# Optimization experiments

Measured on AMD Instinct MI355X. Metric: run time of the kernel, lower is better.

Reference implementation:

```python
import jax, jax.numpy as jnp
import numpy as np

NEG_BIG = -9e15
LRELU_SLOPE = 0.2  # torch LeakyReLU default used for act_att


def setup_inputs() -> dict:
    key = jax.random.key(0)
    k1, k2, k3, k4 = jax.random.split(key, 4)
    B, N, F_in, F_out = 8, 2048, 128, 64
    inp = jax.random.normal(k1, (B, N, F_in), dtype=jnp.float32)
    adj = jax.random.randint(k2, (N, N), 0, 2, dtype=jnp.int32)
    W = jax.random.normal(k3, (F_in, F_out), dtype=jnp.float32) * (1.0 / np.sqrt(F_in))
    a = jax.random.normal(k4, (2 * F_out, 1), dtype=jnp.float32) * (1.0 / np.sqrt(2 * F_out))
    return {"input": inp, "adj": adj, "W": W, "a": a}


def reference(input, adj, W, a):
    # h: [B, N, F_out]
    h = jnp.einsum('bnf,fo->bno', input, W)
    F_out = W.shape[1]
    a1 = a[:F_out, 0]   # [F_out] -- applied to source node i
    a2 = a[F_out:, 0]   # [F_out] -- applied to target node j
    # e[b,i,j] = leaky_relu(h_i . a1 + h_j . a2); equivalent to cat([h_i,h_j]) @ a
    s1 = h @ a1          # [B, N]
    s2 = h @ a2          # [B, N]
    e = jax.nn.leaky_relu(s1[:, :, None] + s2[:, None, :], negative_slope=LRELU_SLOPE)
    masked = jnp.where(adj[None, :, :] > 0, e, NEG_BIG)
    attention = jax.nn.softmax(masked, axis=-1)  # [B, N, N]
    # dropout p=0.0 (eval) -> identity
    h_prime = jnp.einsum('bij,bjo->bio', attention, h)
    out = jax.nn.relu(h_prime)  # concat=True -> apply act_gat
    return out, attention[..., None]
```

## Files before the change

kernel.cpp:

```cpp
#include <hip/hip_runtime.h>
#include <hip/hip_bf16.h>

constexpr int B = 8, N = 2048, FIN = 128, FOUT = 64;

typedef __attribute__((ext_vector_type(8))) short short8;
typedef __attribute__((ext_vector_type(4))) float f32x4;

__device__ __forceinline__ unsigned int pk_bf16(float lo, float hi) {
    union { __hip_bfloat162 h2; unsigned int u; } c;
    c.h2 = __float22bfloat162_rn(float2{lo, hi});
    return c.u;
}
__device__ __forceinline__ unsigned short f2bf(float f) {
    return (unsigned short)(pk_bf16(f, 0.f) & 0xFFFFu);
}

__global__ __launch_bounds__(512, 2) void kA(
        const float* __restrict__ inp, const float* __restrict__ W,
        const float* __restrict__ a, const int* __restrict__ adj,
        unsigned short* __restrict__ hP, float* __restrict__ s1,
        float* __restrict__ s2, unsigned long long* __restrict__ adjbits) {
    __shared__ float wa1l[128], wa2l[128];
    __shared__ unsigned short wT[64][136];
    __shared__ unsigned short aT[128][136];

    int bx = blockIdx.x, t = threadIdx.x, w = t >> 6, lane = t & 63;

    if (bx >= 128) {
        int row = (bx - 128) * 8 + w;
        const int* ar = adj + (size_t)row * N;
        unsigned long long* br = adjbits + (size_t)row * 32;
        #pragma unroll 8
        for (int wq = 0; wq < 32; ++wq) {
            unsigned long long m = __ballot(ar[wq * 64 + lane] > 0);
            if (lane == 0) br[wq] = m;
        }
        return;
    }

    int b = bx >> 4, i0 = (bx & 15) * 128;

    if (t < 128) {
        const float* wr = W + t * FOUT;
        float acc1 = 0.f;
        #pragma unroll 16
        for (int o = 0; o < 64; ++o) acc1 = fmaf(wr[o], a[o], acc1);
        wa1l[t] = acc1;
    } else if (t < 256) {
        int k = t - 128;
        const float* wr = W + k * FOUT;
        float acc2 = 0.f;
        #pragma unroll 16
        for (int o = 0; o < 64; ++o) acc2 = fmaf(wr[o], a[64 + o], acc2);
        wa2l[k] = acc2;
    } else {
        int t2 = t - 256;
        int o = t2 & 63, kg = t2 >> 6;
        #pragma unroll 8
        for (int kk = 0; kk < 32; ++kk) {
            int k = kg * 32 + kk;
            wT[o][k] = f2bf(W[k * FOUT + o]);
        }
    }
    __syncthreads();

    {
        int row = t >> 2, seg = t & 3;
        const float* ip = inp + ((size_t)b * N + i0 + row) * FIN + seg * 32;
        float s1p = 0.f, s2p = 0.f;
        #pragma unroll
        for (int q = 0; q < 8; ++q) {
            float4 v = *(const float4*)&ip[q * 4];
            int k = seg * 32 + q * 4;
            s1p += v.x * wa1l[k] + v.y * wa1l[k + 1] + v.z * wa1l[k + 2] + v.w * wa1l[k + 3];
            s2p += v.x * wa2l[k] + v.y * wa2l[k + 1] + v.z * wa2l[k + 2] + v.w * wa2l[k + 3];
            unsigned int* dst = (unsigned int*)&aT[row][k];
            dst[0] = pk_bf16(v.x, v.y);
            dst[1] = pk_bf16(v.z, v.w);
        }
        s1p += __shfl_xor(s1p, 1); s1p += __shfl_xor(s1p, 2);
        s2p += __shfl_xor(s2p, 1); s2p += __shfl_xor(s2p, 2);
        if (seg == 0) {
            s1[(size_t)b * N + i0 + row] = s1p;
            s2[(size_t)b * N + i0 + row] = s2p;
        }
    }
    __syncthreads();

    int r = lane & 15, g = lane >> 4;
    int mloc = w * 16;
    f32x4 acc[4];
    #pragma unroll
    for (int nf = 0; nf < 4; ++nf)
        #pragma unroll
        for (int q = 0; q < 4; ++q) acc[nf][q] = 0.f;
    #pragma unroll
    for (int ks = 0; ks < 4; ++ks) {
        short8 Af = *(const short8*)&aT[mloc + r][ks * 32 + g * 8];
        #pragma unroll
        for (int nf = 0; nf < 4; ++nf) {
            short8 Bf = *(const short8*)&wT[nf * 16 + r][ks * 32 + g * 8];
            acc[nf] = __builtin_amdgcn_mfma_f32_16x16x32_bf16(Af, Bf, acc[nf], 0, 0, 0);
        }
    }
    __syncthreads();

    #pragma unroll
    for (int nf = 0; nf < 4; ++nf)
        #pragma unroll
        for (int q = 0; q < 4; ++q)
            aT[mloc + g * 4 + q][nf * 16 + r] = f2bf(acc[nf][q]);
    __syncthreads();

    #pragma unroll
    for (int half = 0; half < 2; ++half) {
        int idx = t + half * 512;
        int kb_l = idx >> 8, nf = (idx >> 6) & 3, ln = idx & 63;
        int g2 = ln >> 4, r2 = ln & 15;
        union { short8 s8; unsigned short u[8]; } tw;
        #pragma unroll
        for (int e = 0; e < 8; ++e)
            tw.u[e] = aT[kb_l * 32 + g2 * 8 + e][nf * 16 + r2];
        int kbg = (bx & 15) * 4 + kb_l;
        *(short8*)&hP[((((size_t)b * 64 + kbg) * 4 + nf) << 9) + ln * 8] = tw.s8;
    }
}

__global__ __launch_bounds__(512, 8) void k2a_pv(
        const float* __restrict__ s1g, const float* __restrict__ s2g,
        const unsigned long long* __restrict__ adjbits,
        const unsigned short* __restrict__ hP,
        float* __restrict__ rvg, float* __restrict__ out) {
    __shared__ float s2l[N];
    __shared__ float s1l[16];
    __shared__ float ps[8][16];
    __shared__ float rvl[16];
    __shared__ float red[7][16][68];

    int b = blockIdx.y, m0 = blockIdx.x * 16;
    int t = threadIdx.x, kc = t >> 6, lane = t & 63;
    int r = lane & 15, g = lane >> 4;

    { int j = t * 4; *(float4*)&s2l[j] = *(const float4*)&s2g[(size_t)b * N + j]; }
    if (t < 16) s1l[t] = s1g[(size_t)b * N + m0 + t];
    __syncthreads();

    float s1v = s1l[r];
    const unsigned long long* brow = adjbits + (size_t)(m0 + r) * 32 + kc * 4;
    const unsigned short* hpb = hP + (size_t)b * 64 * 4 * 512;

    f32x4 acc[4];
    #pragma unroll
    for (int nf = 0; nf < 4; ++nf)
        #pragma unroll
        for (int q = 0; q < 4; ++q) acc[nf][q] = 0.f;
    float rsum = 0.f;

    #pragma unroll
    for (int st = 0; st < 8; ++st) {
        int jb = kc * 256 + st * 32 + g * 8;
        unsigned int bits = (unsigned int)(brow[st >> 1] >> ((st & 1) * 32 + g * 8)) & 0xFFu;
        float4 sA = *(const float4*)&s2l[jb];
        float4 sB = *(const float4*)&s2l[jb + 4];
        float sj[8] = {sA.x, sA.y, sA.z, sA.w, sB.x, sB.y, sB.z, sB.w};
        float e8[8];
        #pragma unroll
        for (int e = 0; e < 8; ++e) {
            float x = s1v + sj[e];
            x = fmaxf(x, 0.2f * x);
            float pe = __expf(x);
            e8[e] = ((bits >> e) & 1u) ? pe : 0.f;
            rsum += e8[e];
        }
        union { short8 s8; unsigned int d[4]; } pk;
        #pragma unroll
        for (int e = 0; e < 4; ++e) pk.d[e] = pk_bf16(e8[2 * e], e8[2 * e + 1]);
        int kb = kc * 8 + st;
        const unsigned short* hs = hpb + (((size_t)kb * 4) << 9) + lane * 8;
        #pragma unroll
        for (int nf = 0; nf < 4; ++nf) {
            short8 Bf = *(const short8*)&hs[nf << 9];
            acc[nf] = __builtin_amdgcn_mfma_f32_16x16x32_bf16(pk.s8, Bf, acc[nf], 0, 0, 0);
        }
    }
    rsum += __shfl_xor(rsum, 16);
    rsum += __shfl_xor(rsum, 32);
    if (lane < 16) ps[kc][r] = rsum;
    if (kc > 0) {
        #pragma unroll
        for (int nf = 0; nf < 4; ++nf)
            #pragma unroll
            for (int q = 0; q < 4; ++q)
                red[kc - 1][4 * g + q][nf * 16 + r] = acc[nf][q];
    }
    __syncthreads();
    if (t < 16) {
        float rv = 1.0f / (ps[0][t] + ps[1][t] + ps[2][t] + ps[3][t]
                         + ps[4][t] + ps[5][t] + ps[6][t] + ps[7][t]);
        rvl[t] = rv;
        rvg[(size_t)b * N + m0 + t] = rv;
    }
    __syncthreads();
    if (kc == 0) {
        #pragma unroll
        for (int nf = 0; nf < 4; ++nf) {
            #pragma unroll
            for (int q = 0; q < 4; ++q) {
                int m = 4 * g + q;
                int o = nf * 16 + r;
                float vv = acc[nf][q];
                #pragma unroll
                for (int z = 0; z < 7; ++z) vv += red[z][m][o];
                vv *= rvl[m];
                out[((size_t)b * N + m0 + m) * FOUT + o] = vv > 0.f ? vv : 0.f;
            }
        }
    }
}

__global__ __launch_bounds__(256, 8) void k2b_att(
        const float* __restrict__ s1g, const float* __restrict__ s2g,
        const unsigned long long* __restrict__ adjbits,
        const float* __restrict__ rvg, float* __restrict__ att) {
    int i = blockIdx.x;
    int t = threadIdx.x, w = t >> 6, lane = t & 63;
    int b = blockIdx.y * 4 + w;
    const unsigned long long* brow = adjbits + (size_t)i * 32;
    float s1v = s1g[(size_t)b * N + i];
    float rv  = rvg[(size_t)b * N + i];
    const float* s2b = s2g + (size_t)b * N;
    float* orow = att + ((size_t)b * N + i) * N;
    #pragma unroll
    for (int it = 0; it < 8; ++it) {
        int j = it * 256 + lane * 4;
        unsigned int bits = (unsigned int)(brow[j >> 6] >> (j & 63)) & 0xFu;
        float4 sv = *(const float4*)&s2b[j];
        float x0 = s1v + sv.x; x0 = fmaxf(x0, 0.2f * x0);
        float x1 = s1v + sv.y; x1 = fmaxf(x1, 0.2f * x1);
        float x2 = s1v + sv.z; x2 = fmaxf(x2, 0.2f * x2);
        float x3 = s1v + sv.w; x3 = fmaxf(x3, 0.2f * x3);
        float4 o;
        o.x = (bits & 1u) ? __expf(x0) * rv : 0.f;
        o.y = (bits & 2u) ? __expf(x1) * rv : 0.f;
        o.z = (bits & 4u) ? __expf(x2) * rv : 0.f;
        o.w = (bits & 8u) ? __expf(x3) * rv : 0.f;
        *(float4*)&orow[j] = o;
    }
}

extern "C" void kernel_launch(void* const* d_in, const int* in_sizes, int n_in,
                              void* d_out, int out_size, void* d_ws, size_t ws_size,
                              hipStream_t stream) {
    const float* inp = (const float*)d_in[0];
    const int*   adj = (const int*)d_in[1];
    const float* W   = (const float*)d_in[2];
    const float* a   = (const float*)d_in[3];

    float* out = (float*)d_out;
    float* att = out + (size_t)B * N * FOUT;

    unsigned short* hP = (unsigned short*)d_ws;
    float* s1  = (float*)(hP + (size_t)B * FOUT * N);
    float* s2  = s1 + (size_t)B * N;
    float* rvg = s2 + (size_t)B * N;
    unsigned long long* adjbits = (unsigned long long*)(rvg + (size_t)B * N);

    kA<<<384, 512, 0, stream>>>(inp, W, a, adj, hP, s1, s2, adjbits);
    dim3 g2a(N / 16, B);
    k2a_pv<<<g2a, 512, 0, stream>>>(s1, s2, adjbits, hP, rvg, out);
    dim3 g2b(N, 2);
    k2b_att<<<g2b, 256, 0, stream>>>(s1, s2, adjbits, rvg, att);
}
```

Before: 63.41 us.

## Merge PV and attention-write kernels into one interleaved launch, recomputing row sums

The separate PV and attention-materialisation kernels are combined into one launch of 3072 blocks. Two of every three blocks write attention rows; each computes its own softmax denominator with a first pass of exp over the row before writing, so it no longer depends on the PV kernel's reciprocal. The third block in each group does the PV MFMA work. This removes a launch and the rvg dependency and lets the store-bound attention writes overlap the compute-bound PV, at the cost of computing exp twice per attention element.

Measured after the change: 86.35 us. 36.2% more time.

```diff
diff --git a/kernel.cpp b/kernel.cpp
--- a/kernel.cpp
+++ b/kernel.cpp
@@ -126,19 +126,67 @@
     }
 }
 
-__global__ __launch_bounds__(512, 8) void k2a_pv(
+__global__ __launch_bounds__(512, 8) void k2(
         const float* __restrict__ s1g, const float* __restrict__ s2g,
         const unsigned long long* __restrict__ adjbits,
         const unsigned short* __restrict__ hP,
-        float* __restrict__ rvg, float* __restrict__ out) {
+        float* __restrict__ att, float* __restrict__ out) {
     __shared__ float s2l[N];
     __shared__ float s1l[16];
     __shared__ float ps[8][16];
     __shared__ float rvl[16];
     __shared__ float red[7][16][68];
 
-    int b = blockIdx.y, m0 = blockIdx.x * 16;
-    int t = threadIdx.x, kc = t >> 6, lane = t & 63;
+    int bx = blockIdx.x;
+    int t = threadIdx.x, w = t >> 6, lane = t & 63;
+
+    if (bx % 3 != 2) {
+        int i = (bx / 3) * 2 + (bx % 3);
+        int b = w;
+        const unsigned long long* brow = adjbits + (size_t)i * 32;
+        float s1v = s1g[(size_t)b * N + i];
+        const float* s2b = s2g + (size_t)b * N;
+        float* orow = att + ((size_t)b * N + i) * N;
+        float rsum = 0.f;
+        #pragma unroll
+        for (int it = 0; it < 8; ++it) {
+            int j = it * 256 + lane * 4;
+            unsigned int bits = (unsigned int)(brow[j >> 6] >> (j & 63)) & 0xFu;
+            float4 sv = *(const float4*)&s2b[j];
+            float x0 = s1v + sv.x; x0 = fmaxf(x0, 0.2f * x0);
+            float x1 = s1v + sv.y; x1 = fmaxf(x1, 0.2f * x1);
+            float x2 = s1v + sv.z; x2 = fmaxf(x2, 0.2f * x2);
+            float x3 = s1v + sv.w; x3 = fmaxf(x3, 0.2f * x3);
+            rsum += (bits & 1u) ? __expf(x0) : 0.f;
+            rsum += (bits & 2u) ? __expf(x1) : 0.f;
+            rsum += (bits & 4u) ? __expf(x2) : 0.f;
+            rsum += (bits & 8u) ? __expf(x3) : 0.f;
+        }
+        #pragma unroll
+        for (int off = 1; off < 64; off <<= 1) rsum += __shfl_xor(rsum, off);
+        float rv = 1.0f / rsum;
+        #pragma unroll
+        for (int it = 0; it < 8; ++it) {
+            int j = it * 256 + lane * 4;
+            unsigned int bits = (unsigned int)(brow[j >> 6] >> (j & 63)) & 0xFu;
+            float4 sv = *(const float4*)&s2b[j];
+            float x0 = s1v + sv.x; x0 = fmaxf(x0, 0.2f * x0);
+            float x1 = s1v + sv.y; x1 = fmaxf(x1, 0.2f * x1);
+            float x2 = s1v + sv.z; x2 = fmaxf(x2, 0.2f * x2);
+            float x3 = s1v + sv.w; x3 = fmaxf(x3, 0.2f * x3);
+            float4 o;
+            o.x = (bits & 1u) ? __expf(x0) * rv : 0.f;
+            o.y = (bits & 2u) ? __expf(x1) * rv : 0.f;
+            o.z = (bits & 4u) ? __expf(x2) * rv : 0.f;
+            o.w = (bits & 8u) ? __expf(x3) * rv : 0.f;
+            *(float4*)&orow[j] = o;
+        }
+        return;
+    }
+
+    int pvi = bx / 3;
+    int b = pvi >> 7, m0 = (pvi & 127) * 16;
+    int kc = w;
     int r = lane & 15, g = lane >> 4;
 
     { int j = t * 4; *(float4*)&s2l[j] = *(const float4*)&s2g[(size_t)b * N + j]; }
@@ -194,12 +242,9 @@
                 red[kc - 1][4 * g + q][nf * 16 + r] = acc[nf][q];
     }
     __syncthreads();
-    if (t < 16) {
-        float rv = 1.0f / (ps[0][t] + ps[1][t] + ps[2][t] + ps[3][t]
-                         + ps[4][t] + ps[5][t] + ps[6][t] + ps[7][t]);
-        rvl[t] = rv;
-        rvg[(size_t)b * N + m0 + t] = rv;
-    }
+    if (t < 16)
+        rvl[t] = 1.0f / (ps[0][t] + ps[1][t] + ps[2][t] + ps[3][t]
+                       + ps[4][t] + ps[5][t] + ps[6][t] + ps[7][t]);
     __syncthreads();
     if (kc == 0) {
         #pragma unroll
@@ -218,36 +263,6 @@
     }
 }
 
-__global__ __launch_bounds__(256, 8) void k2b_att(
-        const float* __restrict__ s1g, const float* __restrict__ s2g,
-        const unsigned long long* __restrict__ adjbits,
-        const float* __restrict__ rvg, float* __restrict__ att) {
-    int i = blockIdx.x;
-    int t = threadIdx.x, w = t >> 6, lane = t & 63;
-    int b = blockIdx.y * 4 + w;
-    const unsigned long long* brow = adjbits + (size_t)i * 32;
-    float s1v = s1g[(size_t)b * N + i];
-    float rv  = rvg[(size_t)b * N + i];
-    const float* s2b = s2g + (size_t)b * N;
-    float* orow = att + ((size_t)b * N + i) * N;
-    #pragma unroll
-    for (int it = 0; it < 8; ++it) {
-        int j = it * 256 + lane * 4;
-        unsigned int bits = (unsigned int)(brow[j >> 6] >> (j & 63)) & 0xFu;
-        float4 sv = *(const float4*)&s2b[j];
-        float x0 = s1v + sv.x; x0 = fmaxf(x0, 0.2f * x0);
-        float x1 = s1v + sv.y; x1 = fmaxf(x1, 0.2f * x1);
-        float x2 = s1v + sv.z; x2 = fmaxf(x2, 0.2f * x2);
-        float x3 = s1v + sv.w; x3 = fmaxf(x3, 0.2f * x3);
-        float4 o;
-        o.x = (bits & 1u) ? __expf(x0) * rv : 0.f;
-        o.y = (bits & 2u) ? __expf(x1) * rv : 0.f;
-        o.z = (bits & 4u) ? __expf(x2) * rv : 0.f;
-        o.w = (bits & 8u) ? __expf(x3) * rv : 0.f;
-        *(float4*)&orow[j] = o;
-    }
-}
-
 extern "C" void kernel_launch(void* const* d_in, const int* in_sizes, int n_in,
                               void* d_out, int out_size, void* d_ws, size_t ws_size,
                               hipStream_t stream) {
@@ -262,12 +277,8 @@
     unsigned short* hP = (unsigned short*)d_ws;
     float* s1  = (float*)(hP + (size_t)B * FOUT * N);
     float* s2  = s1 + (size_t)B * N;
-    float* rvg = s2 + (size_t)B * N;
-    unsigned long long* adjbits = (unsigned long long*)(rvg + (size_t)B * N);
+    unsigned long long* adjbits = (unsigned long long*)(s2 + (size_t)B * N);
 
     kA<<<384, 512, 0, stream>>>(inp, W, a, adj, hP, s1, s2, adjbits);
-    dim3 g2a(N / 16, B);
-    k2a_pv<<<g2a, 512, 0, stream>>>(s1, s2, adjbits, hP, rvg, out);
-    dim3 g2b(N, 2);
-    k2b_att<<<g2b, 256, 0, stream>>>(s1, s2, adjbits, rvg, att);
-}
+    k2<<<3072, 512, 0, stream>>>(s1, s2, adjbits, hP, att, out);
+}
```
